# Optimization experiments

Measured on AMD Instinct MI355X. Metric: run time of the kernel, lower is better.

Reference implementation:

```python
import jax, jax.numpy as jnp
import numpy as np

HID = 2048
N_HEADS = 16
N_KV = 16
HEAD_DIM = HID // N_HEADS
N_EXP = 8
TOP_K = 2
MOE_I = 1408
SH_I = 5632
EPS = 1e-6
ROPE_THETA = 1e6


def _rms(x, w):
    v = jnp.mean(jnp.square(x), axis=-1, keepdims=True)
    return (x * jax.lax.rsqrt(v + EPS)) * w


def _rope(q, k):
    # q, k: [B, S, H, D]
    S, D = q.shape[1], q.shape[-1]
    inv = 1.0 / (ROPE_THETA ** (jnp.arange(0, D, 2, dtype=jnp.float32) / D))
    freqs = jnp.arange(S, dtype=jnp.float32)[:, None] * inv[None, :]   # [S, D/2]
    emb = jnp.concatenate([freqs, freqs], axis=-1)                      # [S, D]
    cos = jnp.cos(emb)[None, :, None, :]
    sin = jnp.sin(emb)[None, :, None, :]
    def rot(t):
        t1, t2 = t[..., : D // 2], t[..., D // 2:]
        return jnp.concatenate([-t2, t1], axis=-1)
    return q * cos + rot(q) * sin, k * cos + rot(k) * sin


def setup_inputs() -> dict:
    key = jax.random.key(0)
    ks = jax.random.split(key, 20)
    s = 0.02
    d = {
        "x": jax.random.normal(ks[0], (2, 1024, HID), jnp.float32),
        "w_ln1": jnp.ones((HID,), jnp.float32),
        "wq": jax.random.normal(ks[1], (HID, N_HEADS * HEAD_DIM), jnp.float32) * s,
        "bq": jnp.zeros((N_HEADS * HEAD_DIM,), jnp.float32),
        "wk": jax.random.normal(ks[2], (HID, N_KV * HEAD_DIM), jnp.float32) * s,
        "bk": jnp.zeros((N_KV * HEAD_DIM,), jnp.float32),
        "wv": jax.random.normal(ks[3], (HID, N_KV * HEAD_DIM), jnp.float32) * s,
        "bv": jnp.zeros((N_KV * HEAD_DIM,), jnp.float32),
        "wo": jax.random.normal(ks[4], (N_HEADS * HEAD_DIM, HID), jnp.float32) * s,
        "w_ln2": jnp.ones((HID,), jnp.float32),
        "w_router": jax.random.normal(ks[5], (HID, N_EXP), jnp.float32) * s,
        "w_gate_e": jax.random.normal(ks[6], (N_EXP, HID, MOE_I), jnp.float32) * s,
        "w_up_e": jax.random.normal(ks[7], (N_EXP, HID, MOE_I), jnp.float32) * s,
        "w_down_e": jax.random.normal(ks[8], (N_EXP, MOE_I, HID), jnp.float32) * s,
        "w_sh_gate": jax.random.normal(ks[9], (HID, SH_I), jnp.float32) * s,
        "w_sh_up": jax.random.normal(ks[10], (HID, SH_I), jnp.float32) * s,
        "w_sh_down": jax.random.normal(ks[11], (SH_I, HID), jnp.float32) * s,
        "w_sh_eg": jax.random.normal(ks[12], (HID, 1), jnp.float32) * s,
    }
    return d


def reference(x, w_ln1, wq, bq, wk, bk, wv, bv, wo, w_ln2, w_router,
              w_gate_e, w_up_e, w_down_e, w_sh_gate, w_sh_up, w_sh_down, w_sh_eg):
    B, S, H = x.shape
    # ---- self-attention (pre-norm) ----
    h = _rms(x, w_ln1)
    q = (h @ wq + bq).reshape(B, S, N_HEADS, HEAD_DIM)
    k = (h @ wk + bk).reshape(B, S, N_KV, HEAD_DIM)
    v = (h @ wv + bv).reshape(B, S, N_KV, HEAD_DIM)
    q, k = _rope(q, k)
    rep = N_HEADS // N_KV
    if rep > 1:
        k = jnp.repeat(k, rep, axis=2)
        v = jnp.repeat(v, rep, axis=2)
    scores = jnp.einsum("bqhd,bkhd->bhqk", q, k) * (HEAD_DIM ** -0.5)
    causal = jnp.tril(jnp.ones((S, S), bool))
    scores = jnp.where(causal[None, None], scores, jnp.finfo(scores.dtype).min)
    attn = jax.nn.softmax(scores, axis=-1)
    ctx = jnp.einsum("bhqk,bkhd->bqhd", attn, v).reshape(B, S, N_HEADS * HEAD_DIM)
    x = x + ctx @ wo

    # ---- sparse MoE FFN (pre-norm) ----
    h = _rms(x, w_ln2).reshape(B * S, H)                     # [T, H]
    logits = h @ w_router                                     # [T, E]
    probs = jax.nn.softmax(logits, axis=-1)
    top_w, top_i = jax.lax.top_k(probs, TOP_K)               # norm_topk_prob=False
    combine = jnp.sum(jax.nn.one_hot(top_i, N_EXP, dtype=h.dtype)
                      * top_w[..., None], axis=1)            # [T, E]
    # dense per-expert compute combined with routing weights (same math as
    # the sorted grouped-GEMM dispatch in Qwen2MoeMLPStack)
    g = jnp.einsum("th,ehi->eti", h, w_gate_e)               # [E, T, I]
    u = jnp.einsum("th,ehi->eti", h, w_up_e)
    y = jnp.einsum("eti,eih->eth", jax.nn.silu(g) * u, w_down_e)
    routed = jnp.einsum("eth,te->th", y, combine)            # [T, H]
    # shared expert with sigmoid gate
    sh = (jax.nn.silu(h @ w_sh_gate) * (h @ w_sh_up)) @ w_sh_down
    sh = sh * jax.nn.sigmoid(h @ w_sh_eg)
    x = x + (routed + sh).reshape(B, S, H)
    return x
```

## Files before the change

### kernel.cpp

```cpp
#include <hip/hip_runtime.h>
#include <hip/hip_bf16.h>
#include <math.h>

#define TOKENS 2048
#define HIDDEN 2048
#define NH 16
#define HD 128
#define SEQ 1024
#define MOE_I 1408
#define SH_I 5632
#define K3 6144
#define MAXROWS 5120

typedef __hip_bfloat16 bf16;
typedef short bf16x8 __attribute__((ext_vector_type(8)));
typedef short bf16x4 __attribute__((ext_vector_type(4)));
typedef float f32x4 __attribute__((ext_vector_type(4)));
typedef float f32x16 __attribute__((ext_vector_type(16)));

__device__ __forceinline__ float b2f(bf16 x) { return __bfloat162float(x); }
__device__ __forceinline__ bf16 f2b(float x) { return __float2bfloat16(x); }
__device__ __forceinline__ void split2(float v, short& hi, short& lo) {
    bf16 h = f2b(v);
    bf16 l = f2b(v - b2f(h));
    hi = __builtin_bit_cast(short, h); lo = __builtin_bit_cast(short, l);
}

__device__ __forceinline__ void load_lds16(const void* g, void* l) {
    __builtin_amdgcn_global_load_lds(
        (const __attribute__((address_space(1))) unsigned int*)g,
        (__attribute__((address_space(3))) unsigned int*)l, 16, 0, 0);
}

__global__ __launch_bounds__(256) void rmsnorm3_k(
    const float* __restrict__ x, const float* __restrict__ w, bf16* __restrict__ out)
{
    const int row = blockIdx.x, tid = threadIdx.x;
    const float4* xr = (const float4*)(x + (size_t)row * HIDDEN);
    float4 v1 = xr[tid], v2 = xr[tid + 256];
    float ss = v1.x*v1.x + v1.y*v1.y + v1.z*v1.z + v1.w*v1.w
             + v2.x*v2.x + v2.y*v2.y + v2.z*v2.z + v2.w*v2.w;
    #pragma unroll
    for (int off = 1; off < 64; off <<= 1) ss += __shfl_xor(ss, off);
    __shared__ float ps[4];
    if ((tid & 63) == 0) ps[tid >> 6] = ss;
    __syncthreads();
    float tot = ps[0] + ps[1] + ps[2] + ps[3];
    float r = rsqrtf(tot * (1.0f / HIDDEN) + 1e-6f);
    bf16* o = out + (size_t)row * 4096;
    float vv[8] = {v1.x, v1.y, v1.z, v1.w, v2.x, v2.y, v2.z, v2.w};
    int idx[8]  = {tid*4, tid*4+1, tid*4+2, tid*4+3,
                   1024+tid*4, 1024+tid*4+1, 1024+tid*4+2, 1024+tid*4+3};
    #pragma unroll
    for (int u = 0; u < 8; u++) {
        short hi, lo; split2(vv[u] * r * w[idx[u]], hi, lo);
        o[idx[u]]        = __builtin_bit_cast(bf16, hi);
        o[2048 + idx[u]] = __builtin_bit_cast(bf16, lo);
    }
}

__global__ __launch_bounds__(256) void transpose_wz(
    const float* __restrict__ W, bf16* __restrict__ Wt, int K, int N,
    int nOff, long zsrc, long zdst)
{
    __shared__ float t[32][33];
    W  += (size_t)blockIdx.z * zsrc;
    Wt += (size_t)blockIdx.z * zdst;
    const int n0 = blockIdx.x * 32, k0 = blockIdx.y * 32;
    const int tx = threadIdx.x & 31, ty = threadIdx.x >> 5;
    #pragma unroll
    for (int i = 0; i < 4; i++)
        t[ty + i*8][tx] = W[(size_t)(k0 + ty + i*8) * N + n0 + tx];
    __syncthreads();
    #pragma unroll
    for (int i = 0; i < 4; i++)
        Wt[(size_t)(nOff + n0 + ty + i*8) * K + k0 + tx] = f2b(t[tx][ty + i*8]);
}

__global__ __launch_bounds__(256) void transpose_qkvo_k(
    const float* __restrict__ wq, const float* __restrict__ wk,
    const float* __restrict__ wv, const float* __restrict__ wo,
    bf16* __restrict__ wtqkv, bf16* __restrict__ wt3o)
{
    const int z = blockIdx.z;
    const float* W = (z == 0) ? wq : (z == 1) ? wk : (z == 2) ? wv : wo;
    bf16* Wt2 = (z < 3) ? wtqkv : wt3o;
    const int nOff = (z < 3) ? z * 2048 : 0;
    __shared__ float t[32][33];
    const int n0 = blockIdx.x * 32, k0 = blockIdx.y * 32;
    const int tx = threadIdx.x & 31, ty = threadIdx.x >> 5;
    #pragma unroll
    for (int i = 0; i < 4; i++)
        t[ty + i*8][tx] = W[(size_t)(k0 + ty + i*8) * 2048 + n0 + tx];
    __syncthreads();
    #pragma unroll
    for (int i = 0; i < 4; i++) {
        float v = t[tx][ty + i*8];
        short hi, lo; split2(v, hi, lo);
        bf16* o = Wt2 + (size_t)(nOff + n0 + ty + i*8) * 4096 + k0 + tx;
        o[0]    = __builtin_bit_cast(bf16, hi);
        o[2048] = __builtin_bit_cast(bf16, lo);
    }
}

__global__ __launch_bounds__(256) void transpose_moegu_k(
    const float* __restrict__ ge, const float* __restrict__ ue, bf16* __restrict__ wtgu)
{
    const int z = blockIdx.z, e = z & 7;
    const float* W = ((z < 8) ? ge : ue) + (size_t)e * HIDDEN * MOE_I;
    bf16* Wt = wtgu + (size_t)e * 2816 * HIDDEN;
    const int nOff = (z < 8) ? 0 : MOE_I;
    __shared__ float t[32][33];
    const int n0 = blockIdx.x * 32, k0 = blockIdx.y * 32;
    const int tx = threadIdx.x & 31, ty = threadIdx.x >> 5;
    #pragma unroll
    for (int i = 0; i < 4; i++)
        t[ty + i*8][tx] = W[(size_t)(k0 + ty + i*8) * MOE_I + n0 + tx];
    __syncthreads();
    #pragma unroll
    for (int i = 0; i < 4; i++)
        Wt[(size_t)(nOff + n0 + ty + i*8) * HIDDEN + k0 + tx] = f2b(t[tx][ty + i*8]);
}

__global__ __launch_bounds__(256) void transpose_shgu_k(
    const float* __restrict__ sg, const float* __restrict__ su, bf16* __restrict__ dst)
{
    const int z = blockIdx.z;
    const float* W = z ? su : sg;
    const int nOff = z * SH_I;
    __shared__ float t[32][33];
    const int n0 = blockIdx.x * 32, k0 = blockIdx.y * 32;
    const int tx = threadIdx.x & 31, ty = threadIdx.x >> 5;
    #pragma unroll
    for (int i = 0; i < 4; i++)
        t[ty + i*8][tx] = W[(size_t)(k0 + ty + i*8) * SH_I + n0 + tx];
    __syncthreads();
    #pragma unroll
    for (int i = 0; i < 4; i++)
        dst[(size_t)(nOff + n0 + ty + i*8) * HIDDEN + k0 + tx] = f2b(t[tx][ty + i*8]);
}

__global__ __launch_bounds__(256) void gemm_bt(
    const bf16* __restrict__ A, const bf16* __restrict__ Bt,
    float* __restrict__ Cf, bf16* __restrict__ Cb, const float* __restrict__ bias,
    int M, int N, int K, int ldA, int ldB, int ldC, long zCstride, int limb3, int epi)
{
    __shared__ __align__(16) bf16 As[128 * 64];
    __shared__ __align__(16) bf16 Bs[128 * 64];
    const int tid = threadIdx.x;
    const int lane = tid & 63, wid = tid >> 6;
    const int l32 = lane & 31, lh2 = lane >> 5;
    const int wr = wid >> 1, wc = wid & 1;
    int lid = blockIdx.y * gridDim.x + blockIdx.x;
    {
        const int nwg = gridDim.x * gridDim.y;
        const int q = nwg >> 3, r = nwg & 7;
        const int xcd = lid & 7, idx = lid >> 3;
        lid = (xcd < r ? xcd * (q + 1) : r * (q + 1) + (xcd - r) * q) + idx;
    }
    const int m0 = (lid % gridDim.x) * 128, n0 = (lid / gridDim.x) * 128;
    const int koff = blockIdx.z * K;

    int srow[4], sslot[4];
    #pragma unroll
    for (int i = 0; i < 4; i++) {
        const int c = tid + 256*i;
        srow[i]  = c >> 3;
        sslot[i] = (((c & 7) ^ (srow[i] & 7)) << 3);
    }

    f32x16 acc[2][2];
    #pragma unroll
    for (int m = 0; m < 2; m++)
        #pragma unroll
        for (int n = 0; n < 2; n++)
            #pragma unroll
            for (int j = 0; j < 16; j++) acc[m][n][j] = 0.f;

    for (int k0 = 0; k0 < K; k0 += 64) {
        const int kcat = koff + k0;
        int ka = kcat, kb = kcat;
        if (limb3) {
            ka = (kcat >= 4096) ? kcat - 4096 : kcat;
            kb = (kcat >= 2048) ? kcat - 2048 : kcat;
        }
        __syncthreads();
        #pragma unroll
        for (int i = 0; i < 4; i++) {
            load_lds16(A  + (size_t)(m0 + srow[i]) * ldA + ka + sslot[i], As + (tid + 256*i) * 8);
            load_lds16(Bt + (size_t)(n0 + srow[i]) * ldB + kb + sslot[i], Bs + (tid + 256*i) * 8);
        }
        __syncthreads();
        bf16x8 a[2][4], b[2][4];
        #pragma unroll
        for (int m = 0; m < 2; m++) {
            const int r = wr*64 + m*32 + l32, rx = r & 7;
            #pragma unroll
            for (int kk = 0; kk < 4; kk++)
                a[m][kk] = *(const bf16x8*)&As[r*64 + ((((kk<<1)|lh2) ^ rx) << 3)];
        }
        #pragma unroll
        for (int n = 0; n < 2; n++) {
            const int r = wc*64 + n*32 + l32, rx = r & 7;
            #pragma unroll
            for (int kk = 0; kk < 4; kk++)
                b[n][kk] = *(const bf16x8*)&Bs[r*64 + ((((kk<<1)|lh2) ^ rx) << 3)];
        }
        #pragma unroll
        for (int kk = 0; kk < 4; kk++)
            #pragma unroll
            for (int m = 0; m < 2; m++)
                #pragma unroll
                for (int n = 0; n < 2; n++)
                    acc[m][n] = __builtin_amdgcn_mfma_f32_32x32x16_bf16(a[m][kk], b[n][kk], acc[m][n], 0, 0, 0);
    }

    float* Cz = Cf + (size_t)blockIdx.z * zCstride;
    #pragma unroll
    for (int m = 0; m < 2; m++) {
        const int base_m = m0 + wr*64 + m*32 + 4*lh2;
        #pragma unroll
        for (int n = 0; n < 2; n++) {
            const int gcol = n0 + wc*64 + n*32 + l32;
            #pragma unroll
            for (int reg = 0; reg < 16; reg++) {
                const int grow = base_m + (reg & 3) + 8*(reg >> 2);
                const size_t o = (size_t)grow * ldC + gcol;
                const float v = acc[m][n][reg];
                if (epi == 0)      Cb[o] = f2b(v);
                else if (epi == 4) Cz[o] = v;
                else               Cf[o] = v + bias[gcol];
            }
        }
    }
}

__global__ __launch_bounds__(256) void gemm_gu(
    const bf16* __restrict__ A, const bf16* __restrict__ BtAll,
    const int* __restrict__ offc, const int* __restrict__ perm,
    bf16* __restrict__ C)
{
    const int e = blockIdx.z;
    const int off = offc[8 + e];
    const int padCnt = offc[9 + e] - off;
    const int m0 = blockIdx.x * 128;
    if (m0 >= padCnt) return;
    __shared__ __align__(16) bf16 As[128 * 64];
    __shared__ __align__(16) bf16 Bs[128 * 64];
    const int tid = threadIdx.x;
    const int lane = tid & 63, wid = tid >> 6;
    const int l32 = lane & 31, lh2 = lane >> 5;
    const int wr = wid >> 1, wc = wid & 1;
    const int n0 = blockIdx.y * 128;
    const bf16* Bt = BtAll + (size_t)e * 2816 * 2048;

    int srow[4], sslot[4], tok[4];
    #pragma unroll
    for (int i = 0; i < 4; i++) {
        const int c = tid + 256*i;
        srow[i]  = c >> 3;
        sslot[i] = (((c & 7) ^ (srow[i] & 7)) << 3);
        int t = perm[off + m0 + srow[i]];
        tok[i] = (t < 0) ? 0 : t;
    }

    f32x16 acc[2][2];
    #pragma unroll
    for (int m = 0; m < 2; m++)
        #pragma unroll
        for (int n = 0; n < 2; n++)
            #pragma unroll
            for (int j = 0; j < 16; j++) acc[m][n][j] = 0.f;

    for (int k0 = 0; k0 < 2048; k0 += 64) {
        __syncthreads();
        #pragma unroll
        for (int i = 0; i < 4; i++) {
            load_lds16(A  + (size_t)tok[i] * 2048 + k0 + sslot[i], As + (tid + 256*i) * 8);
            load_lds16(Bt + (size_t)(n0 + srow[i]) * 2048 + k0 + sslot[i], Bs + (tid + 256*i) * 8);
        }
        __syncthreads();
        bf16x8 a[2][4], b[2][4];
        #pragma unroll
        for (int m = 0; m < 2; m++) {
            const int r = wr*64 + m*32 + l32, rx = r & 7;
            #pragma unroll
            for (int kk = 0; kk < 4; kk++)
                a[m][kk] = *(const bf16x8*)&As[r*64 + ((((kk<<1)|lh2) ^ rx) << 3)];
        }
        #pragma unroll
        for (int n = 0; n < 2; n++) {
            const int r = wc*64 + n*32 + l32, rx = r & 7;
            #pragma unroll
            for (int kk = 0; kk < 4; kk++)
                b[n][kk] = *(const bf16x8*)&Bs[r*64 + ((((kk<<1)|lh2) ^ rx) << 3)];
        }
        #pragma unroll
        for (int kk = 0; kk < 4; kk++)
            #pragma unroll
            for (int m = 0; m < 2; m++)
                #pragma unroll
                for (int n = 0; n < 2; n++)
                    acc[m][n] = __builtin_amdgcn_mfma_f32_32x32x16_bf16(a[m][kk], b[n][kk], acc[m][n], 0, 0, 0);
    }

    #pragma unroll
    for (int m = 0; m < 2; m++) {
        const int base_m = m0 + wr*64 + m*32 + 4*lh2;
        #pragma unroll
        for (int n = 0; n < 2; n++) {
            const int gcol = n0 + wc*64 + n*32 + l32;
            #pragma unroll
            for (int reg = 0; reg < 16; reg++) {
                const int grow = base_m + (reg & 3) + 8*(reg >> 2);
                C[(size_t)(off + grow) * 2816 + gcol] = f2b(acc[m][n][reg]);
            }
        }
    }
}

__global__ __launch_bounds__(256) void gemm_down(
    const bf16* __restrict__ A, const bf16* __restrict__ BtAll,
    const int* __restrict__ offc, bf16* __restrict__ Y)
{
    const int e = blockIdx.z;
    const int off = offc[8 + e];
    const int padCnt = offc[9 + e] - off;
    const int m0 = blockIdx.x * 128;
    if (m0 >= padCnt) return;
    __shared__ __align__(16) bf16 As[128 * 64];
    __shared__ __align__(16) bf16 Bs[128 * 64];
    const int tid = threadIdx.x;
    const int lane = tid & 63, wid = tid >> 6;
    const int l32 = lane & 31, lh2 = lane >> 5;
    const int wr = wid >> 1, wc = wid & 1;
    const int n0 = blockIdx.y * 128;
    const bf16* Bt = BtAll + (size_t)e * 2048 * 1408;

    int srow[4], sslot[4];
    #pragma unroll
    for (int i = 0; i < 4; i++) {
        const int c = tid + 256*i;
        srow[i]  = c >> 3;
        sslot[i] = (((c & 7) ^ (srow[i] & 7)) << 3);
    }

    f32x16 acc[2][2];
    #pragma unroll
    for (int m = 0; m < 2; m++)
        #pragma unroll
        for (int n = 0; n < 2; n++)
            #pragma unroll
            for (int j = 0; j < 16; j++) acc[m][n][j] = 0.f;

    for (int k0 = 0; k0 < 1408; k0 += 64) {
        __syncthreads();
        #pragma unroll
        for (int i = 0; i < 4; i++) {
            load_lds16(A  + (size_t)(off + m0 + srow[i]) * 1408 + k0 + sslot[i], As + (tid + 256*i) * 8);
            load_lds16(Bt + (size_t)(n0 + srow[i]) * 1408 + k0 + sslot[i], Bs + (tid + 256*i) * 8);
        }
        __syncthreads();
        bf16x8 a[2][4], b[2][4];
        #pragma unroll
        for (int m = 0; m < 2; m++) {
            const int r = wr*64 + m*32 + l32, rx = r & 7;
            #pragma unroll
            for (int kk = 0; kk < 4; kk++)
                a[m][kk] = *(const bf16x8*)&As[r*64 + ((((kk<<1)|lh2) ^ rx) << 3)];
        }
        #pragma unroll
        for (int n = 0; n < 2; n++) {
            const int r = wc*64 + n*32 + l32, rx = r & 7;
            #pragma unroll
            for (int kk = 0; kk < 4; kk++)
                b[n][kk] = *(const bf16x8*)&Bs[r*64 + ((((kk<<1)|lh2) ^ rx) << 3)];
        }
        #pragma unroll
        for (int kk = 0; kk < 4; kk++)
            #pragma unroll
            for (int m = 0; m < 2; m++)
                #pragma unroll
                for (int n = 0; n < 2; n++)
                    acc[m][n] = __builtin_amdgcn_mfma_f32_32x32x16_bf16(a[m][kk], b[n][kk], acc[m][n], 0, 0, 0);
    }

    #pragma unroll
    for (int m = 0; m < 2; m++) {
        const int base_m = m0 + wr*64 + m*32 + 4*lh2;
        #pragma unroll
        for (int n = 0; n < 2; n++) {
            const int gcol = n0 + wc*64 + n*32 + l32;
            #pragma unroll
            for (int reg = 0; reg < 16; reg++) {
                const int grow = base_m + (reg & 3) + 8*(reg >> 2);
                Y[(size_t)(off + grow) * 2048 + gcol] = f2b(acc[m][n][reg]);
            }
        }
    }
}

__global__ void rope_table_k(float2* __restrict__ cs)
{
    const int i = blockIdx.x * 256 + threadIdx.x;
    const int s = i >> 6, d = i & 63;
    const float fr = (float)s * powf(1.0e6f, -(float)d * (1.0f / 64.0f));
    float c, sn;
    sincosf(fr, &sn, &c);
    cs[i] = make_float2(c, sn);
}

__global__ void rope_f32_k(float* __restrict__ qkv, const float2* __restrict__ cs)
{
    const int idx = blockIdx.x * 256 + threadIdx.x;
    const int d  = idx & 63;
    const int hh = (idx >> 6) & 15;
    const size_t base = (size_t)(idx >> 10) * 6144 + hh * HD;
    const int s = (idx >> 10) & 1023;
    const float2 t = cs[(s << 6) | d];
    const float c = t.x, sn = t.y;
    float q0 = qkv[base + d], q1 = qkv[base + d + 64];
    qkv[base + d]      = q0 * c - q1 * sn;
    qkv[base + d + 64] = q1 * c + q0 * sn;
    float k0 = qkv[base + 2048 + d], k1 = qkv[base + 2048 + d + 64];
    qkv[base + 2048 + d]      = k0 * c - k1 * sn;
    qkv[base + 2048 + d + 64] = k1 * c + k0 * sn;
}

__global__ __launch_bounds__(256) void transpose_v3_k(
    const float* __restrict__ qkv, bf16* __restrict__ vth, bf16* __restrict__ vtl)
{
    __shared__ float t[32][33];
    const int s0 = blockIdx.x * 32, d0 = blockIdx.y * 32;
    const int bh = blockIdx.z, b = bh >> 4, h = bh & 15;
    const int tx = threadIdx.x & 31, ty = threadIdx.x >> 5;
    const float* vb = qkv + ((size_t)b * SEQ) * 6144 + 4096 + h * HD;
    #pragma unroll
    for (int i = 0; i < 4; i++)
        t[ty + i*8][tx] = vb[(size_t)(s0 + ty + i*8) * 6144 + d0 + tx];
    __syncthreads();
    const size_t ob = ((size_t)bh * HD) * SEQ;
    #pragma unroll
    for (int i = 0; i < 4; i++) {
        float val = t[tx][ty + i*8];
        short hi, lo; split2(val, hi, lo);
        const size_t o = ob + (size_t)(d0 + ty + i*8) * SEQ + s0 + tx;
        vth[o] = __builtin_bit_cast(bf16, hi);
        vtl[o] = __builtin_bit_cast(bf16, lo);
    }
}

__global__ __launch_bounds__(256) void attn3_k(
    const float* __restrict__ qkv,
    const bf16* __restrict__ vthg, const bf16* __restrict__ vtlg,
    bf16* __restrict__ ctx2)
{
    __shared__ __align__(16) bf16 SM[32768];
    bf16* Ksh = SM;
    bf16* Ksl = SM + 8192;
    bf16* Vth = SM + 16384;
    bf16* Vtl = SM + 24576;
    bf16* Ph  = SM;
    bf16* Pl  = SM + 4096;

    const int tid = threadIdx.x, lane = tid & 63, wid = tid >> 6;
    const int l16 = lane & 15, lh = lane >> 4;
    const int bh = blockIdx.y, b = bh >> 4, h = bh & 15;
    const int qbase = blockIdx.x * 64;
    const int qw = qbase + wid * 16;
    const float* qp = qkv + ((size_t)b * SEQ) * 6144 + h * HD;
    const float* kp = qkv + ((size_t)b * SEQ) * 6144 + 2048 + h * HD;
    const bf16* vph = vthg + ((size_t)bh * HD) * SEQ;
    const bf16* vpl = vtlg + ((size_t)bh * HD) * SEQ;

    bf16x8 aqh[4], aql[4];
    #pragma unroll
    for (int c = 0; c < 4; c++) {
        const float* qrow = qp + (size_t)(qw + l16) * 6144 + c*32 + lh*8;
        #pragma unroll
        for (int u = 0; u < 8; u++) {
            short hi, lo; split2(qrow[u], hi, lo);
            aqh[c][u] = hi; aql[c][u] = lo;
        }
    }

    f32x4 o[8];
    #pragma unroll
    for (int n = 0; n < 8; n++) o[n] = (f32x4){0.f, 0.f, 0.f, 0.f};
    float mj[4], lj[4];
    #pragma unroll
    for (int j = 0; j < 4; j++) { mj[j] = -1e30f; lj[j] = 0.f; }

    const int kr = tid >> 2;
    const int kc = (tid & 3) * 32;
    const int krx = kr & 15;
    const int kt_end = blockIdx.x + 1;
    for (int kt = 0; kt < kt_end; ++kt) {
        const int kv0 = kt * 64;
        __syncthreads();
        {
            const float* krow = kp + (size_t)(kv0 + kr) * 6144 + kc;
            #pragma unroll
            for (int u = 0; u < 8; u++) {
                float4 kv4 = *(const float4*)(krow + u*4);
                short h0, l0, h1, l1, h2s, l2s, h3, l3;
                split2(kv4.x, h0, l0); split2(kv4.y, h1, l1);
                split2(kv4.z, h2s, l2s); split2(kv4.w, h3, l3);
                bf16x4 h4, l4;
                h4[0] = h0; h4[1] = h1; h4[2] = h2s; h4[3] = h3;
                l4[0] = l0; l4[1] = l1; l4[2] = l2s; l4[3] = l3;
                const int s = (((kc + u*4) >> 3) ^ krx);
                const int dst = kr*128 + (s << 3) + ((u & 1) * 4);
                *(bf16x4*)&Ksh[dst] = h4;
                *(bf16x4*)&Ksl[dst] = l4;
            }
        }
        #pragma unroll
        for (int i = 0; i < 4; i++) {
            const int c = tid + 256*i;
            const int row = c >> 3, sl = (c & 7) ^ (row & 7);
            load_lds16(vph + (size_t)row * SEQ + kv0 + (sl << 3), Vth + c*8);
            load_lds16(vpl + (size_t)row * SEQ + kv0 + (sl << 3), Vtl + c*8);
        }
        __syncthreads();

        f32x4 sg[4];
        #pragma unroll
        for (int g = 0; g < 4; g++) sg[g] = (f32x4){0.f,0.f,0.f,0.f};
        #pragma unroll
        for (int c = 0; c < 4; c++) {
            #pragma unroll
            for (int g = 0; g < 4; g++) {
                const int row = l16 + g*16;
                const int sl = (((c*4 + lh) ^ (row & 15)) << 3);
                bf16x8 bkh = *(const bf16x8*)&Ksh[row*128 + sl];
                bf16x8 bkl = *(const bf16x8*)&Ksl[row*128 + sl];
                sg[g] = __builtin_amdgcn_mfma_f32_16x16x32_bf16(aqh[c], bkh, sg[g], 0, 0, 0);
                sg[g] = __builtin_amdgcn_mfma_f32_16x16x32_bf16(aql[c], bkh, sg[g], 0, 0, 0);
                sg[g] = __builtin_amdgcn_mfma_f32_16x16x32_bf16(aqh[c], bkl, sg[g], 0, 0, 0);
            }
        }
        __syncthreads();

        const float scale = 0.08838834764831845f;
        #pragma unroll
        for (int j = 0; j < 4; j++) {
            const int qrow = qw + lh*4 + j;
            float sv[4];
            #pragma unroll
            for (int g = 0; g < 4; g++) {
                sv[g] = sg[g][j] * scale;
                if (kv0 + l16 + g*16 > qrow) sv[g] = -1e30f;
            }
            float mx = fmaxf(fmaxf(sv[0], sv[1]), fmaxf(sv[2], sv[3]));
            #pragma unroll
            for (int off = 1; off < 16; off <<= 1) mx = fmaxf(mx, __shfl_xor(mx, off, 16));
            const float nm = fmaxf(mj[j], mx);
            const float al = __expf(mj[j] - nm);
            float pg[4], rs = 0.f;
            #pragma unroll
            for (int g = 0; g < 4; g++) { pg[g] = __expf(sv[g] - nm); rs += pg[g]; }
            #pragma unroll
            for (int off = 1; off < 16; off <<= 1) rs += __shfl_xor(rs, off, 16);
            lj[j] = lj[j] * al + rs;
            mj[j] = nm;
            #pragma unroll
            for (int n = 0; n < 8; n++) o[n][j] *= al;
            const int prow = lh*4 + j;
            #pragma unroll
            for (int g = 0; g < 4; g++) {
                short hi, lo; split2(pg[g], hi, lo);
                const int col = l16 + g*16;
                const int addr = wid*1024 + prow*64 + ((((col >> 3) ^ (prow & 7)) << 3)) + (col & 7);
                Ph[addr] = __builtin_bit_cast(bf16, hi);
                Pl[addr] = __builtin_bit_cast(bf16, lo);
            }
        }
        #pragma unroll
        for (int ks = 0; ks < 2; ks++) {
            const int psl = (((ks*4 + lh) ^ (l16 & 7)) << 3);
            bf16x8 aph = *(const bf16x8*)&Ph[wid*1024 + l16*64 + psl];
            bf16x8 apl = *(const bf16x8*)&Pl[wid*1024 + l16*64 + psl];
            #pragma unroll
            for (int n = 0; n < 8; n++) {
                const int row = n*16 + l16;
                const int vsl = (((ks*4 + lh) ^ (row & 7)) << 3);
                bf16x8 bvh = *(const bf16x8*)&Vth[row*64 + vsl];
                bf16x8 bvl = *(const bf16x8*)&Vtl[row*64 + vsl];
                o[n] = __builtin_amdgcn_mfma_f32_16x16x32_bf16(aph, bvh, o[n], 0, 0, 0);
                o[n] = __builtin_amdgcn_mfma_f32_16x16x32_bf16(apl, bvh, o[n], 0, 0, 0);
                o[n] = __builtin_amdgcn_mfma_f32_16x16x32_bf16(aph, bvl, o[n], 0, 0, 0);
            }
        }
    }

    float inv[4];
    #pragma unroll
    for (int j = 0; j < 4; j++) inv[j] = 1.0f / lj[j];
    #pragma unroll
    for (int n = 0; n < 8; n++)
        #pragma unroll
        for (int j = 0; j < 4; j++) {
            const float v = o[n][j] * inv[j];
            short hi, lo; split2(v, hi, lo);
            const size_t base = ((size_t)b * SEQ + (qw + lh*4 + j)) * 4096 + h * HD + n*16 + l16;
            ctx2[base]        = __builtin_bit_cast(bf16, hi);
            ctx2[base + 2048] = __builtin_bit_cast(bf16, lo);
        }
}

__global__ __launch_bounds__(256) void combine_rms_router_k(
    const float* __restrict__ x, const float* __restrict__ xp,
    const float* __restrict__ wln, const float* __restrict__ wr,
    const float* __restrict__ weg,
    float* __restrict__ x1, bf16* __restrict__ h2,
    float* __restrict__ comb, float* __restrict__ sigeg)
{
    const int row = blockIdx.x, tid = threadIdx.x;
    const size_t rb = (size_t)row * HIDDEN;
    const long zs = (long)TOKENS * HIDDEN;
    __shared__ float ps[4];
    __shared__ float pacc[4][9];
    float4 v[2];
    #pragma unroll
    for (int u = 0; u < 2; u++) {
        const int i = tid + u * 256;
        float4 a  = ((const float4*)(x + rb))[i];
        float4 p0 = ((const float4*)(xp + rb))[i];
        float4 p1 = ((const float4*)(xp + zs + rb))[i];
        float4 p2 = ((const float4*)(xp + 2*zs + rb))[i];
        v[u].x = a.x + p0.x + p1.x + p2.x;
        v[u].y = a.y + p0.y + p1.y + p2.y;
        v[u].z = a.z + p0.z + p1.z + p2.z;
        v[u].w = a.w + p0.w + p1.w + p2.w;
        ((float4*)(x1 + rb))[i] = v[u];
    }
    float ss = v[0].x*v[0].x + v[0].y*v[0].y + v[0].z*v[0].z + v[0].w*v[0].w
             + v[1].x*v[1].x + v[1].y*v[1].y + v[1].z*v[1].z + v[1].w*v[1].w;
    #pragma unroll
    for (int off = 1; off < 64; off <<= 1) ss += __shfl_xor(ss, off);
    if ((tid & 63) == 0) ps[tid >> 6] = ss;
    __syncthreads();
    const float tot = ps[0] + ps[1] + ps[2] + ps[3];
    const float r = rsqrtf(tot * (1.0f / HIDDEN) + 1e-6f);

    float acc[9];
// ... 34 lines not shown
        const float invs = 1.0f / s;
        #pragma unroll
        for (int e = 0; e < 8; e++) p[e] *= invs;
        int i1 = 0;
        #pragma unroll
        for (int e = 1; e < 8; e++) if (p[e] > p[i1]) i1 = e;
        int i2 = (i1 == 0) ? 1 : 0;
        #pragma unroll
        for (int e = 0; e < 8; e++) if (e != i1 && p[e] > p[i2]) i2 = e;
        #pragma unroll
        for (int e = 0; e < 8; e++)
            comb[(size_t)row * 8 + e] = (e == i1 || e == i2) ? p[e] : 0.f;
        sigeg[row] = 1.0f / (1.0f + expf(-lg[8]));
    }
}

__global__ __launch_bounds__(256) void count_fill_k(
    const float* __restrict__ comb, int* __restrict__ offc, int* __restrict__ perm,
    float* __restrict__ scale, int* __restrict__ inv)
{
    __shared__ int cnt[8], off[9], fil[8];
    const int tid = threadIdx.x;
    if (tid < 8) { cnt[tid] = 0; fil[tid] = 0; }
    __syncthreads();
    for (int t = tid; t < TOKENS; t += 256)
        #pragma unroll
        for (int e = 0; e < 8; e++)
            if (comb[(size_t)t * 8 + e] > 0.f) atomicAdd(&cnt[e], 1);
    __syncthreads();
    if (tid == 0) {
        off[0] = 0;
        for (int e = 0; e < 8; e++) off[e+1] = off[e] + ((cnt[e] + 127) & ~127);
    }
    __syncthreads();
    for (int i = tid; i < MAXROWS; i += 256) { perm[i] = -1; scale[i] = 0.f; }
    __syncthreads();
    for (int t = tid; t < TOKENS; t += 256) {
        int j = 0;
        #pragma unroll
        for (int e = 0; e < 8; e++) {
            const float c = comb[(size_t)t * 8 + e];
            if (c > 0.f) {
                int s = atomicAdd(&fil[e], 1);
                int slot = off[e] + s;
                perm[slot] = t;
                scale[slot] = c;
                inv[t * 2 + j] = slot;
                j++;
            }
        }
    }
    __syncthreads();
    if (tid < 9) offc[8 + tid] = off[tid];
}

__global__ void silu_k(const bf16* __restrict__ g, bf16* __restrict__ a,
                       const float* __restrict__ rowScale,
                       int I, int ldg, int rowsConst, const int* __restrict__ rowsPtr)
{
    const int idx = (blockIdx.x * 256 + threadIdx.x) * 4;
    const int rows = rowsPtr ? *rowsPtr : rowsConst;
    const int row = idx / I;
    if (row >= rows) return;
    const int col = idx - row * I;
    const float s = rowScale[row];
    const bf16* gr = g + (size_t)row * ldg + col;
    bf16* ar = a + (size_t)row * I + col;
    #pragma unroll
    for (int c = 0; c < 4; c++) {
        const float gv = b2f(gr[c]), uv = b2f(gr[I + c]);
        ar[c] = f2b(s * gv / (1.0f + __expf(-gv)) * uv);
    }
}

__global__ void final_k(const float* __restrict__ x1, const bf16* __restrict__ y,
                        const int* __restrict__ inv, const float* __restrict__ ysh,
                        float* __restrict__ out)
{
    const int i = blockIdx.x * 256 + threadIdx.x;
    const int t = i >> 9;
    const int col = (i & 511) * 4;
    const int s0 = inv[t*2], s1 = inv[t*2 + 1];
    const long zs = (long)TOKENS * HIDDEN;
    float4 a  = ((const float4*)x1)[i];
    float4 h0 = ((const float4*)ysh)[i];
    float4 h1 = ((const float4*)(ysh + zs))[i];
    const bf16* y0 = y + (size_t)s0 * 2048 + col;
    const bf16* y1 = y + (size_t)s1 * 2048 + col;
    float4 r;
    r.x = a.x + h0.x + h1.x + b2f(y0[0]) + b2f(y1[0]);
    r.y = a.y + h0.y + h1.y + b2f(y0[1]) + b2f(y1[1]);
    r.z = a.z + h0.z + h1.z + b2f(y0[2]) + b2f(y1[2]);
    r.w = a.w + h0.w + h1.w + b2f(y0[3]) + b2f(y1[3]);
    ((float4*)out)[i] = r;
}

extern "C" void kernel_launch(void* const* d_in, const int* in_sizes, int n_in,
                              void* d_out, int out_size, void* d_ws, size_t ws_size,
                              hipStream_t stream)
{
    const float* x     = (const float*)d_in[0];
    const float* w_ln1 = (const float*)d_in[1];
    const float* wq    = (const float*)d_in[2];
    const float* bq    = (const float*)d_in[3];
    const float* wk    = (const float*)d_in[4];
    const float* bk    = (const float*)d_in[5];
    const float* wv    = (const float*)d_in[6];
    const float* bv    = (const float*)d_in[7];
    const float* wo    = (const float*)d_in[8];
    const float* w_ln2 = (const float*)d_in[9];
    const float* w_rt  = (const float*)d_in[10];
    const float* w_ge  = (const float*)d_in[11];
    const float* w_ue  = (const float*)d_in[12];
    const float* w_de  = (const float*)d_in[13];
    const float* w_sg  = (const float*)d_in[14];
    const float* w_su  = (const float*)d_in[15];
    const float* w_sd  = (const float*)d_in[16];
    const float* w_eg  = (const float*)d_in[17];
    float* out = (float*)d_out;
    (void)in_sizes; (void)n_in; (void)out_size; (void)ws_size;

    char* ws = (char*)d_ws;
    float* x1    = (float*)(ws + 0);
    bf16*  h2    = (bf16*)(ws + 16777216);
    float* comb  = (float*)(ws + 25165824);
    float* seg   = (float*)(ws + 25231360);
    int*   offc  = (int*)(ws + 25239552);
    float* scale = (float*)(ws + 25243648);
    int*   perm  = (int*)(ws + 25276416);
    int*   inv   = (int*)(ws + 25297920);
    float* bqkv  = (float*)(ws + 25314304);
    float2* ropecs = (float2*)(ws + 25338880);
    const size_t S = 25863168;
    bf16*  hcat  = (bf16*)(ws + S);
    bf16*  wtqkv = (bf16*)(ws + S + 16777216);
    float* qkvf  = (float*)(ws + S + 67108864);
    bf16*  wt3o  = (bf16*)(ws + S + 117440512);
    bf16*  vth   = (bf16*)(ws + S);
    bf16*  vtl   = (bf16*)(ws + S + 8388608);
    bf16*  ctx2  = (bf16*)(ws + S + 16777216);
    float* xp    = (float*)(ws + S + 50331648);
    bf16*  wtgu  = (bf16*)(ws + S);
    bf16*  gb    = (bf16*)(ws + S + 92274688);
    bf16*  ab    = (bf16*)(ws + S);
    bf16*  wtd   = (bf16*)(ws + S + 14417920);
    bf16*  ymoe  = (bf16*)(ws + S + 60555264);
    bf16*  wtshgu = (bf16*)(ws + S);
    bf16*  gsh    = (bf16*)(ws + S + 81526784);
    bf16*  ash    = (bf16*)(ws + S);
    bf16*  wtshd  = (bf16*)(ws + S + 23068672);
    float* ysh    = (float*)(ws + S + 81526784);

    rmsnorm3_k<<<TOKENS, 256, 0, stream>>>(x, w_ln1, hcat);
    (void)hipMemcpyAsync(bqkv,        bq, 8192, hipMemcpyDeviceToDevice, stream);
    (void)hipMemcpyAsync(bqkv + 2048, bk, 8192, hipMemcpyDeviceToDevice, stream);
    (void)hipMemcpyAsync(bqkv + 4096, bv, 8192, hipMemcpyDeviceToDevice, stream);
    rope_table_k<<<256, 256, 0, stream>>>(ropecs);

    transpose_qkvo_k<<<dim3(64, 64, 4), 256, 0, stream>>>(wq, wk, wv, wo, wtqkv, wt3o);
    gemm_bt<<<dim3(16, 48, 1), 256, 0, stream>>>(hcat, wtqkv, qkvf, nullptr, bqkv,
                                                 TOKENS, 6144, K3, 4096, 4096, 6144, 0, 1, 5);

    rope_f32_k<<<8192, 256, 0, stream>>>(qkvf, ropecs);
    transpose_v3_k<<<dim3(32, 4, 32), 256, 0, stream>>>(qkvf, vth, vtl);
    attn3_k<<<dim3(16, 32), 256, 0, stream>>>(qkvf, vth, vtl, ctx2);

    gemm_bt<<<dim3(16, 16, 3), 256, 0, stream>>>(ctx2, wt3o, xp, nullptr, nullptr,
                                                 TOKENS, HIDDEN, 2048, 4096, 4096, 2048,
                                                 (long)TOKENS * HIDDEN, 1, 4);
    combine_rms_router_k<<<TOKENS, 256, 0, stream>>>(x, xp, w_ln2, w_rt, w_eg,
                                                     x1, h2, comb, seg);
    count_fill_k<<<1, 256, 0, stream>>>(comb, offc, perm, scale, inv);

    transpose_moegu_k<<<dim3(44, 64, 16), 256, 0, stream>>>(w_ge, w_ue, wtgu);
    gemm_gu<<<dim3(MAXROWS/128, 22, 8), 256, 0, stream>>>(h2, wtgu, offc, perm, gb);
    silu_k<<<(MAXROWS * MOE_I) / 1024, 256, 0, stream>>>(gb, ab, scale, MOE_I, 2816, 0, offc + 16);
    transpose_wz<<<dim3(64, 44, 8), 256, 0, stream>>>(w_de, wtd, MOE_I, HIDDEN, 0,
                                                      (long)MOE_I*HIDDEN, (long)HIDDEN*MOE_I);
    gemm_down<<<dim3(MAXROWS/128, 16, 8), 256, 0, stream>>>(ab, wtd, offc, ymoe);

    transpose_shgu_k<<<dim3(176, 64, 2), 256, 0, stream>>>(w_sg, w_su, wtshgu);
    gemm_bt<<<dim3(16, 88, 1), 256, 0, stream>>>(h2, wtshgu, nullptr, gsh, nullptr,
                                                 TOKENS, 2*SH_I, HIDDEN, HIDDEN, HIDDEN, 2*SH_I, 0, 0, 0);
    silu_k<<<(TOKENS * SH_I) / 1024, 256, 0, stream>>>(gsh, ash, seg, SH_I, 2*SH_I, TOKENS, nullptr);
    transpose_wz<<<dim3(64, 176, 1), 256, 0, stream>>>(w_sd, wtshd, SH_I, HIDDEN, 0, 0, 0);
    gemm_bt<<<dim3(16, 16, 2), 256, 0, stream>>>(ash, wtshd, ysh, nullptr, nullptr,
                                                 TOKENS, HIDDEN, SH_I/2, SH_I, SH_I, 2048,
                                                 (long)TOKENS * HIDDEN, 0, 4);

    final_k<<<(TOKENS * HIDDEN) / 1024, 256, 0, stream>>>(x1, ymoe, inv, ysh, out);
}
```

Before: 971.6 us.

## Fuse SiLU into gate/up GEMMs, RoPE into attention, widen transposes

Gate and up weight rows are interleaved so each GEMM epilogue pairs gate/up values across adjacent lanes and writes SiLU(g)*u*scale directly. This removes the separate silu kernels and the wide intermediate buffers, for both the MoE and the shared expert. RoPE is applied inside the attention kernel while loading Q and K, which drops the standalone rope pass. All weight transposes now use 64x64 tiles with float4 loads and 4-wide bf16 stores, and s_setprio hints are added around the MFMA sections in attention. The risks are extra shuffles and half-idle lanes in the epilogue, plus RoPE work repeated per K tile in attention.

Result: no change. 980.0 us (+0.9%).

```diff
diff --git a/kernel.cpp b/kernel.cpp
--- a/kernel.cpp
+++ b/kernel.cpp
@@ -59,22 +59,33 @@
     }
 }
 
-__global__ __launch_bounds__(256) void transpose_wz(
+__global__ __launch_bounds__(256) void transpose64_k(
     const float* __restrict__ W, bf16* __restrict__ Wt, int K, int N,
-    int nOff, long zsrc, long zdst)
-{
-    __shared__ float t[32][33];
+    long zsrc, long zdst)
+{
+    __shared__ float t[64][65];
     W  += (size_t)blockIdx.z * zsrc;
     Wt += (size_t)blockIdx.z * zdst;
-    const int n0 = blockIdx.x * 32, k0 = blockIdx.y * 32;
-    const int tx = threadIdx.x & 31, ty = threadIdx.x >> 5;
-    #pragma unroll
-    for (int i = 0; i < 4; i++)
-        t[ty + i*8][tx] = W[(size_t)(k0 + ty + i*8) * N + n0 + tx];
-    __syncthreads();
-    #pragma unroll
-    for (int i = 0; i < 4; i++)
-        Wt[(size_t)(nOff + n0 + ty + i*8) * K + k0 + tx] = f2b(t[tx][ty + i*8]);
+    const int n0 = blockIdx.x * 64, k0 = blockIdx.y * 64;
+    const int tid = threadIdx.x;
+    #pragma unroll
+    for (int i = 0; i < 4; i++) {
+        const int idx = tid + 256*i;
+        const int r = idx >> 4, q = idx & 15;
+        float4 v = *(const float4*)(W + (size_t)(k0 + r) * N + n0 + q*4);
+        t[r][q*4+0] = v.x; t[r][q*4+1] = v.y; t[r][q*4+2] = v.z; t[r][q*4+3] = v.w;
+    }
+    __syncthreads();
+    #pragma unroll
+    for (int i = 0; i < 4; i++) {
+        const int idx = tid + 256*i;
+        const int nl = idx >> 4, kc = idx & 15;
+        bf16x4 o4;
+        #pragma unroll
+        for (int j = 0; j < 4; j++)
+            o4[j] = __builtin_bit_cast(short, f2b(t[kc*4+j][nl]));
+        *(bf16x4*)(Wt + (size_t)(n0 + nl) * K + k0 + kc*4) = o4;
+    }
 }
 
 __global__ __launch_bounds__(256) void transpose_qkvo_k(
@@ -86,63 +97,94 @@
     const float* W = (z == 0) ? wq : (z == 1) ? wk : (z == 2) ? wv : wo;
     bf16* Wt2 = (z < 3) ? wtqkv : wt3o;
     const int nOff = (z < 3) ? z * 2048 : 0;
-    __shared__ float t[32][33];
-    const int n0 = blockIdx.x * 32, k0 = blockIdx.y * 32;
-    const int tx = threadIdx.x & 31, ty = threadIdx.x >> 5;
-    #pragma unroll
-    for (int i = 0; i < 4; i++)
-        t[ty + i*8][tx] = W[(size_t)(k0 + ty + i*8) * 2048 + n0 + tx];
-    __syncthreads();
-    #pragma unroll
-    for (int i = 0; i < 4; i++) {
-        float v = t[tx][ty + i*8];
-        short hi, lo; split2(v, hi, lo);
-        bf16* o = Wt2 + (size_t)(nOff + n0 + ty + i*8) * 4096 + k0 + tx;
-        o[0]    = __builtin_bit_cast(bf16, hi);
-        o[2048] = __builtin_bit_cast(bf16, lo);
+    __shared__ float t[64][65];
+    const int n0 = blockIdx.x * 64, k0 = blockIdx.y * 64;
+    const int tid = threadIdx.x;
+    #pragma unroll
+    for (int i = 0; i < 4; i++) {
+        const int idx = tid + 256*i;
+        const int r = idx >> 4, q = idx & 15;
+        float4 v = *(const float4*)(W + (size_t)(k0 + r) * 2048 + n0 + q*4);
+        t[r][q*4+0] = v.x; t[r][q*4+1] = v.y; t[r][q*4+2] = v.z; t[r][q*4+3] = v.w;
+    }
+    __syncthreads();
+    #pragma unroll
+    for (int i = 0; i < 4; i++) {
+        const int idx = tid + 256*i;
+        const int nl = idx >> 4, kc = idx & 15;
+        bf16x4 h4, l4;
+        #pragma unroll
+        for (int j = 0; j < 4; j++) {
+            short hi, lo; split2(t[kc*4+j][nl], hi, lo);
+            h4[j] = hi; l4[j] = lo;
+        }
+        bf16* o = Wt2 + (size_t)(nOff + n0 + nl) * 4096 + k0 + kc*4;
+        *(bf16x4*)o = h4;
+        *(bf16x4*)(o + 2048) = l4;
     }
 }
 
 __global__ __launch_bounds__(256) void transpose_moegu_k(
     const float* __restrict__ ge, const float* __restrict__ ue, bf16* __restrict__ wtgu)
 {
-    const int z = blockIdx.z, e = z & 7;
-    const float* W = ((z < 8) ? ge : ue) + (size_t)e * HIDDEN * MOE_I;
+    const int z = blockIdx.z, e = z & 7, isUp = z >> 3;
+    const float* W = (isUp ? ue : ge) + (size_t)e * HIDDEN * MOE_I;
     bf16* Wt = wtgu + (size_t)e * 2816 * HIDDEN;
-    const int nOff = (z < 8) ? 0 : MOE_I;
-    __shared__ float t[32][33];
-    const int n0 = blockIdx.x * 32, k0 = blockIdx.y * 32;
-    const int tx = threadIdx.x & 31, ty = threadIdx.x >> 5;
-    #pragma unroll
-    for (int i = 0; i < 4; i++)
-        t[ty + i*8][tx] = W[(size_t)(k0 + ty + i*8) * MOE_I + n0 + tx];
-    __syncthreads();
-    #pragma unroll
-    for (int i = 0; i < 4; i++)
-        Wt[(size_t)(nOff + n0 + ty + i*8) * HIDDEN + k0 + tx] = f2b(t[tx][ty + i*8]);
+    __shared__ float t[64][65];
+    const int n0 = blockIdx.x * 64, k0 = blockIdx.y * 64;
+    const int tid = threadIdx.x;
+    #pragma unroll
+    for (int i = 0; i < 4; i++) {
+        const int idx = tid + 256*i;
+        const int r = idx >> 4, q = idx & 15;
+        float4 v = *(const float4*)(W + (size_t)(k0 + r) * MOE_I + n0 + q*4);
+        t[r][q*4+0] = v.x; t[r][q*4+1] = v.y; t[r][q*4+2] = v.z; t[r][q*4+3] = v.w;
+    }
+    __syncthreads();
+    #pragma unroll
+    for (int i = 0; i < 4; i++) {
+        const int idx = tid + 256*i;
+        const int nl = idx >> 4, kc = idx & 15;
+        bf16x4 o4;
+        #pragma unroll
+        for (int j = 0; j < 4; j++)
+            o4[j] = __builtin_bit_cast(short, f2b(t[kc*4+j][nl]));
+        *(bf16x4*)(Wt + (size_t)(2*(n0 + nl) + isUp) * 2048 + k0 + kc*4) = o4;
+    }
 }
 
 __global__ __launch_bounds__(256) void transpose_shgu_k(
     const float* __restrict__ sg, const float* __restrict__ su, bf16* __restrict__ dst)
 {
-    const int z = blockIdx.z;
-    const float* W = z ? su : sg;
-    const int nOff = z * SH_I;
-    __shared__ float t[32][33];
-    const int n0 = blockIdx.x * 32, k0 = blockIdx.y * 32;
-    const int tx = threadIdx.x & 31, ty = threadIdx.x >> 5;
-    #pragma unroll
-    for (int i = 0; i < 4; i++)
-        t[ty + i*8][tx] = W[(size_t)(k0 + ty + i*8) * SH_I + n0 + tx];
-    __syncthreads();
-    #pragma unroll
-    for (int i = 0; i < 4; i++)
-        dst[(size_t)(nOff + n0 + ty + i*8) * HIDDEN + k0 + tx] = f2b(t[tx][ty + i*8]);
+    const int isUp = blockIdx.z;
+    const float* W = isUp ? su : sg;
+    __shared__ float t[64][65];
+    const int n0 = blockIdx.x * 64, k0 = blockIdx.y * 64;
+    const int tid = threadIdx.x;
+    #pragma unroll
+    for (int i = 0; i < 4; i++) {
+        const int idx = tid + 256*i;
+        const int r = idx >> 4, q = idx & 15;
+        float4 v = *(const float4*)(W + (size_t)(k0 + r) * SH_I + n0 + q*4);
+        t[r][q*4+0] = v.x; t[r][q*4+1] = v.y; t[r][q*4+2] = v.z; t[r][q*4+3] = v.w;
+    }
+    __syncthreads();
+    #pragma unroll
+    for (int i = 0; i < 4; i++) {
+        const int idx = tid + 256*i;
+        const int nl = idx >> 4, kc = idx & 15;
+        bf16x4 o4;
+        #pragma unroll
+        for (int j = 0; j < 4; j++)
+            o4[j] = __builtin_bit_cast(short, f2b(t[kc*4+j][nl]));
+        *(bf16x4*)(dst + (size_t)(2*(n0 + nl) + isUp) * 2048 + k0 + kc*4) = o4;
+    }
 }
 
 __global__ __launch_bounds__(256) void gemm_bt(
     const bf16* __restrict__ A, const bf16* __restrict__ Bt,
     float* __restrict__ Cf, bf16* __restrict__ Cb, const float* __restrict__ bias,
+    const float* __restrict__ rowsc,
     int M, int N, int K, int ldA, int ldB, int ldC, long zCstride, int limb3, int epi)
 {
     __shared__ __align__(16) bf16 As[128 * 64];
@@ -225,11 +267,20 @@
             #pragma unroll
             for (int reg = 0; reg < 16; reg++) {
                 const int grow = base_m + (reg & 3) + 8*(reg >> 2);
-                const size_t o = (size_t)grow * ldC + gcol;
                 const float v = acc[m][n][reg];
-                if (epi == 0)      Cb[o] = f2b(v);
-                else if (epi == 4) Cz[o] = v;
-                else               Cf[o] = v + bias[gcol];
+                if (epi == 6) {
+                    const float pv = __shfl_xor(v, 1);
+                    if (!(l32 & 1)) {
+                        const float g = v, u = pv;
+                        const float y = rowsc[grow] * g / (1.0f + __expf(-g)) * u;
+                        Cb[(size_t)grow * ldC + (gcol >> 1)] = f2b(y);
+                    }
+                } else {
+                    const size_t o = (size_t)grow * ldC + gcol;
+                    if (epi == 0)      Cb[o] = f2b(v);
+                    else if (epi == 4) Cz[o] = v;
+                    else               Cf[o] = v + bias[gcol];
+                }
             }
         }
     }
@@ -238,7 +289,7 @@
 __global__ __launch_bounds__(256) void gemm_gu(
     const bf16* __restrict__ A, const bf16* __restrict__ BtAll,
     const int* __restrict__ offc, const int* __restrict__ perm,
-    bf16* __restrict__ C)
+    const float* __restrict__ scale, bf16* __restrict__ AB)
 {
     const int e = blockIdx.z;
     const int off = offc[8 + e];
@@ -313,7 +364,13 @@
             #pragma unroll
             for (int reg = 0; reg < 16; reg++) {
                 const int grow = base_m + (reg & 3) + 8*(reg >> 2);
-                C[(size_t)(off + grow) * 2816 + gcol] = f2b(acc[m][n][reg]);
+                const float v = acc[m][n][reg];
+                const float pv = __shfl_xor(v, 1);
+                if (!(l32 & 1)) {
+                    const float g = v, u = pv;
+                    const float y = scale[off + grow] * g / (1.0f + __expf(-g)) * u;
+                    AB[(size_t)(off + grow) * MOE_I + (gcol >> 1)] = f2b(y);
+                }
             }
         }
     }
@@ -410,23 +467,6 @@
     cs[i] = make_float2(c, sn);
 }
 
-__global__ void rope_f32_k(float* __restrict__ qkv, const float2* __restrict__ cs)
-{
-    const int idx = blockIdx.x * 256 + threadIdx.x;
-    const int d  = idx & 63;
-    const int hh = (idx >> 6) & 15;
-    const size_t base = (size_t)(idx >> 10) * 6144 + hh * HD;
-    const int s = (idx >> 10) & 1023;
-    const float2 t = cs[(s << 6) | d];
-    const float c = t.x, sn = t.y;
-    float q0 = qkv[base + d], q1 = qkv[base + d + 64];
-    qkv[base + d]      = q0 * c - q1 * sn;
-    qkv[base + d + 64] = q1 * c + q0 * sn;
-    float k0 = qkv[base + 2048 + d], k1 = qkv[base + 2048 + d + 64];
-    qkv[base + 2048 + d]      = k0 * c - k1 * sn;
-    qkv[base + 2048 + d + 64] = k1 * c + k0 * sn;
-}
-
 __global__ __launch_bounds__(256) void transpose_v3_k(
     const float* __restrict__ qkv, bf16* __restrict__ vth, bf16* __restrict__ vtl)
 {
@@ -451,7 +491,7 @@
 }
 
 __global__ __launch_bounds__(256) void attn3_k(
-    const float* __restrict__ qkv,
+    const float* __restrict__ qkv, const float2* __restrict__ ropecs,
     const bf16* __restrict__ vthg, const bf16* __restrict__ vtlg,
     bf16* __restrict__ ctx2)
 {
@@ -474,14 +514,32 @@
     const bf16* vpl = vtlg + ((size_t)bh * HD) * SEQ;
 
     bf16x8 aqh[4], aql[4];
-    #pragma unroll
-    for (int c = 0; c < 4; c++) {
-        const float* qrow = qp + (size_t)(qw + l16) * 6144 + c*32 + lh*8;
-        #pragma unroll
-        for (int u = 0; u < 8; u++) {
-            short hi, lo; split2(qrow[u], hi, lo);
-            aqh[c][u] = hi; aql[c][u] = lo;
-        }
+    {
+        float qr[4][8];
+        const int tok = qw + l16;
+        #pragma unroll
+        for (int c = 0; c < 4; c++) {
+            const float* qrow = qp + (size_t)tok * 6144 + c*32 + lh*8;
+            #pragma unroll
+            for (int u = 0; u < 8; u++) qr[c][u] = qrow[u];
+        }
+        #pragma unroll
+        for (int c = 0; c < 2; c++)
+            #pragma unroll
+            for (int u = 0; u < 8; u++) {
+                const int d = c*32 + lh*8 + u;
+                const float2 cs_ = ropecs[(tok << 6) | d];
+                const float a = qr[c][u], bb = qr[c+2][u];
+                qr[c][u]   = a * cs_.x - bb * cs_.y;
+                qr[c+2][u] = bb * cs_.x + a * cs_.y;
+            }
+        #pragma unroll
+        for (int c = 0; c < 4; c++)
+            #pragma unroll
+            for (int u = 0; u < 8; u++) {
+                short hi, lo; split2(qr[c][u], hi, lo);
+                aqh[c][u] = hi; aql[c][u] = lo;
+            }
     }
 
     f32x4 o[8];
@@ -492,27 +550,50 @@
     for (int j = 0; j < 4; j++) { mj[j] = -1e30f; lj[j] = 0.f; }
 
     const int kr = tid >> 2;
-    const int kc = (tid & 3) * 32;
+    const int q16 = tid & 3;
     const int krx = kr & 15;
     const int kt_end = blockIdx.x + 1;
     for (int kt = 0; kt < kt_end; ++kt) {
         const int kv0 = kt * 64;
         __syncthreads();
         {
-            const float* krow = kp + (size_t)(kv0 + kr) * 6144 + kc;
-            #pragma unroll
-            for (int u = 0; u < 8; u++) {
-                float4 kv4 = *(const float4*)(krow + u*4);
-                short h0, l0, h1, l1, h2s, l2s, h3, l3;
-                split2(kv4.x, h0, l0); split2(kv4.y, h1, l1);
-                split2(kv4.z, h2s, l2s); split2(kv4.w, h3, l3);
-                bf16x4 h4, l4;
-                h4[0] = h0; h4[1] = h1; h4[2] = h2s; h4[3] = h3;
-                l4[0] = l0; l4[1] = l1; l4[2] = l2s; l4[3] = l3;
-                const int s = (((kc + u*4) >> 3) ^ krx);
-                const int dst = kr*128 + (s << 3) + ((u & 1) * 4);
-                *(bf16x4*)&Ksh[dst] = h4;
-                *(bf16x4*)&Ksl[dst] = l4;
+            const int tokk = kv0 + kr;
+            const float* krow = kp + (size_t)tokk * 6144;
+            float4 A4[4], B4[4];
+            #pragma unroll
+            for (int u = 0; u < 4; u++) {
+                A4[u] = *(const float4*)(krow + q16*16 + u*4);
+                B4[u] = *(const float4*)(krow + 64 + q16*16 + u*4);
+            }
+            #pragma unroll
+            for (int u = 0; u < 4; u++) {
+                #pragma unroll
+                for (int j = 0; j < 4; j++) {
+                    const int d = q16*16 + u*4 + j;
+                    const float2 cs_ = ropecs[(tokk << 6) | d];
+                    float* pa = ((float*)&A4[u]) + j;
+                    float* pb = ((float*)&B4[u]) + j;
+                    const float a = *pa, bb = *pb;
+                    *pa = a * cs_.x - bb * cs_.y;
+                    *pb = bb * cs_.x + a * cs_.y;
+                }
+                bf16x4 h4, l4, h4b, l4b;
+                #pragma unroll
+                for (int j = 0; j < 4; j++) {
+                    short hi, lo;
+                    split2(((float*)&A4[u])[j], hi, lo); h4[j] = hi; l4[j] = lo;
+                    split2(((float*)&B4[u])[j], hi, lo); h4b[j] = hi; l4b[j] = lo;
+                }
+                const int colA = q16*16 + u*4;
+                const int sA = ((colA >> 3) ^ krx);
+                const int dstA = kr*128 + (sA << 3) + ((u & 1) * 4);
+                *(bf16x4*)&Ksh[dstA] = h4;
+                *(bf16x4*)&Ksl[dstA] = l4;
+                const int colB = 64 + colA;
+                const int sB = ((colB >> 3) ^ krx);
+                const int dstB = kr*128 + (sB << 3) + ((u & 1) * 4);
+                *(bf16x4*)&Ksh[dstB] = h4b;
+                *(bf16x4*)&Ksl[dstB] = l4b;
             }
         }
         #pragma unroll
@@ -527,6 +608,7 @@
         f32x4 sg[4];
         #pragma unroll
         for (int g = 0; g < 4; g++) sg[g] = (f32x4){0.f,0.f,0.f,0.f};
+        __builtin_amdgcn_s_setprio(1);
         #pragma unroll
         for (int c = 0; c < 4; c++) {
             #pragma unroll
@@ -540,6 +622,7 @@
                 sg[g] = __builtin_amdgcn_mfma_f32_16x16x32_bf16(aqh[c], bkl, sg[g], 0, 0, 0);
             }
         }
+        __builtin_amdgcn_s_setprio(0);
         __syncthreads();
 
         const float scale = 0.08838834764831845f;
@@ -576,6 +659,7 @@
                 Pl[addr] = __builtin_bit_cast(bf16, lo);
             }
         }
+        __builtin_amdgcn_s_setprio(1);
         #pragma unroll
         for (int ks = 0; ks < 2; ks++) {
             const int psl = (((ks*4 + lh) ^ (l16 & 7)) << 3);
@@ -592,6 +676,7 @@
                 o[n] = __builtin_amdgcn_mfma_f32_16x16x32_bf16(aph, bvl, o[n], 0, 0, 0);
             }
         }
+        __builtin_amdgcn_s_setprio(0);
     }
 
     float inv[4];
@@ -732,25 +817,6 @@
     }
     __syncthreads();
     if (tid < 9) offc[8 + tid] = off[tid];
-}
-
-__global__ void silu_k(const bf16* __restrict__ g, bf16* __restrict__ a,
-                       const float* __restrict__ rowScale,
-                       int I, int ldg, int rowsConst, const int* __restrict__ rowsPtr)
-{
-    const int idx = (blockIdx.x * 256 + threadIdx.x) * 4;
-    const int rows = rowsPtr ? *rowsPtr : rowsConst;
-    const int row = idx / I;
-    if (row >= rows) return;
-    const int col = idx - row * I;
-    const float s = rowScale[row];
-    const bf16* gr = g + (size_t)row * ldg + col;
-    bf16* ar = a + (size_t)row * I + col;
-    #pragma unroll
-    for (int c = 0; c < 4; c++) {
-        const float gv = b2f(gr[c]), uv = b2f(gr[I + c]);
-        ar[c] = f2b(s * gv / (1.0f + __expf(-gv)) * uv);
-    }
 }
 
 __global__ void final_k(const float* __restrict__ x1, const bf16* __restrict__ y,
@@ -821,15 +887,13 @@
     bf16*  ctx2  = (bf16*)(ws + S + 16777216);
     float* xp    = (float*)(ws + S + 50331648);
     bf16*  wtgu  = (bf16*)(ws + S);
-    bf16*  gb    = (bf16*)(ws + S + 92274688);
-    bf16*  ab    = (bf16*)(ws + S);
-    bf16*  wtd   = (bf16*)(ws + S + 14417920);
-    bf16*  ymoe  = (bf16*)(ws + S + 60555264);
+    bf16*  ab    = (bf16*)(ws + S + 92274688);
+    bf16*  wtd   = (bf16*)(ws + S);
+    bf16*  ymoe  = (bf16*)(ws + S + 46137344);
     bf16*  wtshgu = (bf16*)(ws + S);
-    bf16*  gsh    = (bf16*)(ws + S + 81526784);
-    bf16*  ash    = (bf16*)(ws + S);
-    bf16*  wtshd  = (bf16*)(ws + S + 23068672);
-    float* ysh    = (float*)(ws + S + 81526784);
+    bf16*  ash    = (bf16*)(ws + S + 67108864);
+    bf16*  wtshd  = (bf16*)(ws + S);
+    float* ysh    = (float*)(ws + S + 90177536);
 
     rmsnorm3_k<<<TOKENS, 256, 0, stream>>>(x, w_ln1, hcat);
     (void)hipMemcpyAsync(bqkv,        bq, 8192, hipMemcpyDeviceToDevice, stream);
@@ -837,34 +901,31 @@
     (void)hipMemcpyAsync(bqkv + 4096, bv, 8192, hipMemcpyDeviceToDevice, stream);
     rope_table_k<<<256, 256, 0, stream>>>(ropecs);
 
-    transpose_qkvo_k<<<dim3(64, 64, 4), 256, 0, stream>>>(wq, wk, wv, wo, wtqkv, wt3o);
-    gemm_bt<<<dim3(16, 48, 1), 256, 0, stream>>>(hcat, wtqkv, qkvf, nullptr, bqkv,
+    transpose_qkvo_k<<<dim3(32, 32, 4), 256, 0, stream>>>(wq, wk, wv, wo, wtqkv, wt3o);
+    gemm_bt<<<dim3(16, 48, 1), 256, 0, stream>>>(hcat, wtqkv, qkvf, nullptr, bqkv, nullptr,
                                                  TOKENS, 6144, K3, 4096, 4096, 6144, 0, 1, 5);
 
-    rope_f32_k<<<8192, 256, 0, stream>>>(qkvf, ropecs);
     transpose_v3_k<<<dim3(32, 4, 32), 256, 0, stream>>>(qkvf, vth, vtl);
-    attn3_k<<<dim3(16, 32), 256, 0, stream>>>(qkvf, vth, vtl, ctx2);
-
-    gemm_bt<<<dim3(16, 16, 3), 256, 0, stream>>>(ctx2, wt3o, xp, nullptr, nullptr,
+    attn3_k<<<dim3(16, 32), 256, 0, stream>>>(qkvf, ropecs, vth, vtl, ctx2);
+
+    gemm_bt<<<dim3(16, 16, 3), 256, 0, stream>>>(ctx2, wt3o, xp, nullptr, nullptr, nullptr,
                                                  TOKENS, HIDDEN, 2048, 4096, 4096, 2048,
                                                  (long)TOKENS * HIDDEN, 1, 4);
     combine_rms_router_k<<<TOKENS, 256, 0, stream>>>(x, xp, w_ln2, w_rt, w_eg,
                                                      x1, h2, comb, seg);
     count_fill_k<<<1, 256, 0, stream>>>(comb, offc, perm, scale, inv);
 
-    transpose_moegu_k<<<dim3(44, 64, 16), 256, 0, stream>>>(w_ge, w_ue, wtgu);
-    gemm_gu<<<dim3(MAXROWS/128, 22, 8), 256, 0, stream>>>(h2, wtgu, offc, perm, gb);
-    silu_k<<<(MAXROWS * MOE_I) / 1024, 256, 0, stream>>>(gb, ab, scale, MOE_I, 2816, 0, offc + 16);
-    transpose_wz<<<dim3(64, 44, 8), 256, 0, stream>>>(w_de, wtd, MOE_I, HIDDEN, 0,
-                                                      (long)MOE_I*HIDDEN, (long)HIDDEN*MOE_I);
+    transpose_moegu_k<<<dim3(22, 32, 16), 256, 0, stream>>>(w_ge, w_ue, wtgu);
+    gemm_gu<<<dim3(MAXROWS/128, 22, 8), 256, 0, stream>>>(h2, wtgu, offc, perm, scale, ab);
+    transpose64_k<<<dim3(32, 22, 8), 256, 0, stream>>>(w_de, wtd, MOE_I, HIDDEN,
+                                                       (long)MOE_I*HIDDEN, (long)HIDDEN*MOE_I);
     gemm_down<<<dim3(MAXROWS/128, 16, 8), 256, 0, stream>>>(ab, wtd, offc, ymoe);
 
-    transpose_shgu_k<<<dim3(176, 64, 2), 256, 0, stream>>>(w_sg, w_su, wtshgu);
-    gemm_bt<<<dim3(16, 88, 1), 256, 0, stream>>>(h2, wtshgu, nullptr, gsh, nullptr,
-                                                 TOKENS, 2*SH_I, HIDDEN, HIDDEN, HIDDEN, 2*SH_I, 0, 0, 0);
-    silu_k<<<(TOKENS * SH_I) / 1024, 256, 0, stream>>>(gsh, ash, seg, SH_I, 2*SH_I, TOKENS, nullptr);
-    transpose_wz<<<dim3(64, 176, 1), 256, 0, stream>>>(w_sd, wtshd, SH_I, HIDDEN, 0, 0, 0);
-    gemm_bt<<<dim3(16, 16, 2), 256, 0, stream>>>(ash, wtshd, ysh, nullptr, nullptr,
+    transpose_shgu_k<<<dim3(88, 32, 2), 256, 0, stream>>>(w_sg, w_su, wtshgu);
+    gemm_bt<<<dim3(16, 88, 1), 256, 0, stream>>>(h2, wtshgu, nullptr, ash, nullptr, seg,
+                                                 TOKENS, 2*SH_I, HIDDEN, HIDDEN, HIDDEN, SH_I, 0, 0, 6);
+    transpose64_k<<<dim3(32, 88, 1), 256, 0, stream>>>(w_sd, wtshd, SH_I, HIDDEN, 0, 0);
+    gemm_bt<<<dim3(16, 16, 2), 256, 0, stream>>>(ash, wtshd, ysh, nullptr, nullptr, nullptr,
                                                  TOKENS, HIDDEN, SH_I/2, SH_I, SH_I, 2048,
                                                  (long)TOKENS * HIDDEN, 0, 4);
 
```
